# Kernel optimization log

Hardware: AMD Instinct MI355X
Metric: run time of the kernel (lower is better)

The kernel has to match this reference:

```python
import jax, jax.numpy as jnp
import numpy as np

B, L, DI = 256, 64, 2048   # batch, image regions, image feature dim
T, DT = 32, 512            # caption length, text embedding dim
U, A = 512, 512            # GRU units, attention units


def setup_inputs() -> dict:
    key = jax.random.key(0)
    ks = jax.random.split(key, 14)
    s = 0.02
    return {
        "img": jax.random.normal(ks[0], (B, L, DI), jnp.float32),
        "text": jax.random.normal(ks[1], (B, T, DT), jnp.float32),
        "kernel": jax.random.normal(ks[2], (DI + DT, 3 * U), jnp.float32) * s,
        "input_bias": jax.random.normal(ks[3], (3 * U,), jnp.float32) * s,
        "recurrent_kernel": jax.random.normal(ks[4], (U, 3 * U), jnp.float32) * s,
        "recurrent_bias": jax.random.normal(ks[5], (3 * U,), jnp.float32) * s,
        "att_img_kernel": jax.random.normal(ks[6], (DI, A), jnp.float32) * s,
        "att_img_bias": jax.random.normal(ks[7], (A,), jnp.float32) * s,
        "att_hidden_kernel": jax.random.normal(ks[8], (U, A), jnp.float32) * s,
        "att_hidden_bias": jax.random.normal(ks[9], (A,), jnp.float32) * s,
        "att_v_kernel": jax.random.normal(ks[10], (A, 1), jnp.float32) * s,
        "att_v_bias": jax.random.normal(ks[11], (1,), jnp.float32) * s,
    }


def reference(img, text, kernel, input_bias, recurrent_kernel, recurrent_bias,
              att_img_kernel, att_img_bias, att_hidden_kernel, att_hidden_bias,
              att_v_kernel, att_v_bias):
    # Precompute the image attention projection (independent of h; the
    # original recomputes it each step, but the math is identical).
    img_proj = jnp.einsum('bld,da->bla', img, att_img_kernel) + att_img_bias  # [B,L,A]

    def step(h, x_t):
        # Bahdanau attention over image regions
        hid = jnp.tanh(img_proj + (h @ att_hidden_kernel + att_hidden_bias)[:, None, :])  # [B,L,A]
        score = hid @ att_v_kernel + att_v_bias                # [B,L,1]
        attw = jax.nn.softmax(score, axis=1)                   # softmax over regions
        ctx = jnp.sum(attw * img, axis=1)                      # [B,DI]
        # GRU gate math (keras GRU v2 convention, reset gate applied after matmul)
        inp = jnp.concatenate([x_t, ctx], axis=-1)             # [B,DT+DI]
        mx = inp @ kernel + input_bias                         # [B,3U]
        mi = h @ recurrent_kernel + recurrent_bias             # [B,3U]
        x_z, x_r, x_h = jnp.split(mx, 3, axis=-1)
        r_z, r_r, r_h = jnp.split(mi, 3, axis=-1)
        z = jax.nn.sigmoid(x_z + r_z)
        r = jax.nn.sigmoid(x_r + r_r)
        hh = jnp.tanh(x_h + r * r_h)
        h_new = z * h + (1.0 - z) * hh
        return h_new, h_new

    h0 = jnp.zeros((img.shape[0], recurrent_kernel.shape[0]), img.dtype)
    _, seq = jax.lax.scan(step, h0, jnp.swapaxes(text, 0, 1))  # seq: [T,B,U]
    return jnp.swapaxes(seq, 0, 1)                             # [B,T,U]
```

## Files before the change

kernel.cpp:

```cpp
#include <hip/hip_runtime.h>
#include <hip/hip_bf16.h>

#define B_  256
#define L_  64
#define DI_ 2048
#define T_  32
#define DT_ 512
#define U_  512
#define A_  512
#define N3U 1536

typedef short short8 __attribute__((ext_vector_type(8)));
typedef float floatx4 __attribute__((ext_vector_type(4)));

__device__ __forceinline__ unsigned short f2bf(float f) {
  unsigned int u = __float_as_uint(f);
  u += 0x7fffu + ((u >> 16) & 1u);
  return (unsigned short)(u >> 16);
}
__device__ __forceinline__ float bf2f(unsigned short s) {
  return __uint_as_float(((unsigned int)s) << 16);
}
__device__ __forceinline__ float fast_tanh(float x) {
  x = fminf(fmaxf(x, -15.f), 15.f);
  float e = __expf(2.f * x);
  return (e - 1.f) / (e + 1.f);
}

__global__ __launch_bounds__(256) void gemm_a32_bt16_mfma(
    const float* __restrict__ A, const unsigned short* __restrict__ Bt,
    const float* __restrict__ bias, void* __restrict__ Cout,
    int M, int N, int K, int out_bf16) {
  __shared__ unsigned short As[128][40];
  __shared__ unsigned short Bs[128][40];
  const int tid  = threadIdx.x;
  const int wave = tid >> 6;
  const int lane = tid & 63;
  const int quad = lane >> 4;
  const int lr   = lane & 15;
  const int wrow = (wave >> 1) * 64;
  const int wcol = (wave & 1) * 64;
  const size_t bm = (size_t)blockIdx.y * 128;
  const size_t bn = (size_t)blockIdx.x * 128;

  const int sr = tid >> 2;
  const int sc = (tid & 3) * 8;

  floatx4 acc[4][4] = {};

  for (int k0 = 0; k0 < K; k0 += 32) {
#pragma unroll
    for (int it = 0; it < 2; ++it) {
      const int row = sr + it * 64;
      const float* ap = A + (bm + row) * (size_t)K + k0 + sc;
      float4 a0 = *(const float4*)(ap);
      float4 a1 = *(const float4*)(ap + 4);
      short8 pk;
      pk[0] = (short)f2bf(a0.x); pk[1] = (short)f2bf(a0.y);
      pk[2] = (short)f2bf(a0.z); pk[3] = (short)f2bf(a0.w);
      pk[4] = (short)f2bf(a1.x); pk[5] = (short)f2bf(a1.y);
      pk[6] = (short)f2bf(a1.z); pk[7] = (short)f2bf(a1.w);
      *(short8*)&As[row][sc] = pk;
      *(float4*)&Bs[row][sc] = *(const float4*)(Bt + (bn + row) * (size_t)K + k0 + sc);
    }
    __syncthreads();
    short8 af[4], bf[4];
#pragma unroll
    for (int mi = 0; mi < 4; ++mi) af[mi] = *(const short8*)&As[wrow + mi * 16 + lr][quad * 8];
#pragma unroll
    for (int ni = 0; ni < 4; ++ni) bf[ni] = *(const short8*)&Bs[wcol + ni * 16 + lr][quad * 8];
#pragma unroll
    for (int mi = 0; mi < 4; ++mi)
#pragma unroll
      for (int ni = 0; ni < 4; ++ni)
        acc[mi][ni] = __builtin_amdgcn_mfma_f32_16x16x32_bf16(af[mi], bf[ni], acc[mi][ni], 0, 0, 0);
    __syncthreads();
  }

  float* outf = (float*)Cout;
  unsigned short* outb = (unsigned short*)Cout;
#pragma unroll
  for (int mi = 0; mi < 4; ++mi) {
#pragma unroll
    for (int ni = 0; ni < 4; ++ni) {
      const size_t row0 = bm + wrow + mi * 16 + quad * 4;
      const size_t col  = bn + wcol + ni * 16 + lr;
      const float bsum = bias ? bias[col] : 0.f;
#pragma unroll
      for (int reg = 0; reg < 4; ++reg) {
        const float v = acc[mi][ni][reg] + bsum;
        if (out_bf16) outb[(row0 + reg) * (size_t)N + col] = f2bf(v);
        else          outf[(row0 + reg) * (size_t)N + col] = v;
      }
    }
  }
}

__global__ void zero_f32(float* __restrict__ p, int n) {
  int i = blockIdx.x * 256 + threadIdx.x;
  if (i < n) p[i] = 0.f;
}

__global__ __launch_bounds__(256) void transpose_f32_bf16(
    const float* __restrict__ in, unsigned short* __restrict__ outp, int K, int N) {
  __shared__ unsigned short tile[32][33];
  const int tid = threadIdx.x;
  const int tx = tid & 31, ty = tid >> 5;
  const int k0 = blockIdx.y * 32, n0 = blockIdx.x * 32;
#pragma unroll
  for (int i = 0; i < 4; ++i) {
    const int kk = ty + i * 8;
    tile[tx][kk] = f2bf(in[(size_t)(k0 + kk) * N + n0 + tx]);
  }
  __syncthreads();
#pragma unroll
  for (int i = 0; i < 4; ++i) {
    const int nn = ty + i * 8;
    outp[(size_t)(n0 + nn) * K + k0 + tx] = tile[nn][tx];
  }
}

__global__ void build_bcat(const float* __restrict__ ahb,
                           const float* __restrict__ rb,
                           float* __restrict__ bcat) {
  int i = blockIdx.x * 256 + threadIdx.x;
  if (i < A_) bcat[i] = ahb[i];
  else if (i < A_ + N3U) bcat[i] = rb[i - A_];
}

__global__ __launch_bounds__(512) void attn_gru_step(
    const unsigned short* __restrict__ img_proj,
    const unsigned short* __restrict__ imgW,
    const float* __restrict__ text_proj,
    const float* __restrict__ hm,
    const float* __restrict__ vk,
    float* __restrict__ h,
    float* __restrict__ out,
    int t) {
  const int b = blockIdx.x;
  const int tid = threadIdx.x;
  const int lane = tid & 63;
  const int wave = tid >> 6;
  __shared__ float sc[L_];
  __shared__ float aw[L_];

  const float* hpg = hm + (size_t)b * 2048;
  float hpv[8], vvv[8];
  {
    float4 h0 = *(const float4*)(hpg + lane * 8);
    float4 h1 = *(const float4*)(hpg + lane * 8 + 4);
    float4 v0 = *(const float4*)(vk + lane * 8);
    float4 v1 = *(const float4*)(vk + lane * 8 + 4);
    hpv[0]=h0.x; hpv[1]=h0.y; hpv[2]=h0.z; hpv[3]=h0.w;
    hpv[4]=h1.x; hpv[5]=h1.y; hpv[6]=h1.z; hpv[7]=h1.w;
    vvv[0]=v0.x; vvv[1]=v0.y; vvv[2]=v0.z; vvv[3]=v0.w;
    vvv[4]=v1.x; vvv[5]=v1.y; vvv[6]=v1.z; vvv[7]=v1.w;
  }

#pragma unroll
  for (int i = 0; i < 8; ++i) {
    const int l = wave + i * 8;
    const unsigned short* ip = img_proj + ((size_t)b * L_ + l) * A_ + lane * 8;
    short8 v8 = *(const short8*)ip;
    float s = 0.f;
#pragma unroll
    for (int j = 0; j < 8; ++j) {
      s += fast_tanh(bf2f((unsigned short)v8[j]) + hpv[j]) * vvv[j];
    }
#pragma unroll
    for (int off = 32; off; off >>= 1) s += __shfl_down(s, off);
    if (lane == 0) sc[l] = s;
  }
  __syncthreads();

  if (tid < 64) {
    float x = sc[tid];
    float m = x;
#pragma unroll
    for (int off = 32; off; off >>= 1) m = fmaxf(m, __shfl_xor(m, off));
    float e = __expf(x - m);
    float ssum = e;
#pragma unroll
    for (int off = 32; off; off >>= 1) ssum += __shfl_xor(ssum, off);
    aw[tid] = e / ssum;
  }
  __syncthreads();

  const int u = tid;
  const unsigned short* iw = imgW + (size_t)b * L_ * N3U + u;
  float s0 = 0.f, s1 = 0.f, s2 = 0.f;
#pragma unroll 8
  for (int l = 0; l < L_; ++l) {
    const float a = aw[l];
    const unsigned short* p = iw + l * N3U;
    s0 += a * bf2f(p[0]);
    s1 += a * bf2f(p[512]);
    s2 += a * bf2f(p[1024]);
  }
  const float* tp  = text_proj + ((size_t)b * T_ + t) * N3U;
  const float* mib = hm + (size_t)b * 2048 + 512;
  const float xz = s0 + tp[u]        + mib[u];
  const float xr = s1 + tp[512 + u]  + mib[512 + u];
  const float xh = s2 + tp[1024 + u];
  const float rh = mib[1024 + u];
  const float z = 1.f / (1.f + __expf(-xz));
  const float r = 1.f / (1.f + __expf(-xr));
  const float hh = fast_tanh(xh + r * rh);
  const float hn = z * h[b * U_ + u] + (1.f - z) * hh;
  h[b * U_ + u] = hn;
  out[((size_t)b * T_ + t) * U_ + u] = hn;
}

extern "C" void kernel_launch(void* const* d_in, const int* in_sizes, int n_in,
                              void* d_out, int out_size, void* d_ws, size_t ws_size,
                              hipStream_t stream) {
  const float* img        = (const float*)d_in[0];
  const float* text       = (const float*)d_in[1];
  const float* kern       = (const float*)d_in[2];
  const float* input_bias = (const float*)d_in[3];
  const float* rec_kern   = (const float*)d_in[4];
  const float* rec_bias   = (const float*)d_in[5];
  const float* att_img_k  = (const float*)d_in[6];
  const float* att_img_b  = (const float*)d_in[7];
  const float* att_hid_k  = (const float*)d_in[8];
  const float* att_hid_b  = (const float*)d_in[9];
  const float* att_v_k    = (const float*)d_in[10];
  float* out = (float*)d_out;

  char* ws = (char*)d_ws;
  size_t off = 0;
  auto alloc = [&](size_t bytes) { char* p = ws + off; off += (bytes + 255) & ~(size_t)255; return p; };
  unsigned short* img_proj = (unsigned short*)alloc((size_t)B_*L_*A_*2);
  unsigned short* imgW     = (unsigned short*)alloc((size_t)B_*L_*N3U*2);
  float*          text_proj= (float*)         alloc((size_t)B_*T_*N3U*4);
  unsigned short* wt1      = (unsigned short*)alloc((size_t)A_*DI_*2);
  unsigned short* wt2      = (unsigned short*)alloc((size_t)N3U*DI_*2);
  unsigned short* wt3      = (unsigned short*)alloc((size_t)N3U*DT_*2);
  unsigned short* wcatT    = (unsigned short*)alloc((size_t)2048*U_*2);
  float*          bcat     = (float*)         alloc(2048*4);
  float*          h        = (float*)         alloc((size_t)B_*U_*4);
  float*          hm       = (float*)         alloc((size_t)B_*2048*4);

  dim3 blk(256);

  zero_f32<<<dim3((B_*U_ + 255) / 256), blk, 0, stream>>>(h, B_*U_);

  transpose_f32_bf16<<<dim3(A_/32, DI_/32), blk, 0, stream>>>(att_img_k, wt1, DI_, A_);
  transpose_f32_bf16<<<dim3(N3U/32, DI_/32), blk, 0, stream>>>(kern + (size_t)DT_*N3U, wt2, DI_, N3U);
  transpose_f32_bf16<<<dim3(N3U/32, DT_/32), blk, 0, stream>>>(kern, wt3, DT_, N3U);
  transpose_f32_bf16<<<dim3(A_/32, U_/32), blk, 0, stream>>>(att_hid_k, wcatT, U_, A_);
  transpose_f32_bf16<<<dim3(N3U/32, U_/32), blk, 0, stream>>>(rec_kern, wcatT + (size_t)A_*U_, U_, N3U);
  build_bcat<<<dim3(8), blk, 0, stream>>>(att_hid_b, rec_bias, bcat);

  gemm_a32_bt16_mfma<<<dim3(A_/128, (B_*L_)/128), blk, 0, stream>>>(
      img, wt1, att_img_b, img_proj, B_*L_, A_, DI_, 1);
  gemm_a32_bt16_mfma<<<dim3(N3U/128, (B_*L_)/128), blk, 0, stream>>>(
      img, wt2, nullptr, imgW, B_*L_, N3U, DI_, 1);
  gemm_a32_bt16_mfma<<<dim3(N3U/128, (B_*T_)/128), blk, 0, stream>>>(
      text, wt3, input_bias, text_proj, B_*T_, N3U, DT_, 0);

  for (int t = 0; t < T_; ++t) {
    gemm_a32_bt16_mfma<<<dim3(2048/128, B_/128), blk, 0, stream>>>(
        h, wcatT, bcat, hm, B_, 2048, U_, 0);
    attn_gru_step<<<dim3(B_), dim3(512), 0, stream>>>(
        img_proj, imgW, text_proj, hm, att_v_k, h, out, t);
  }
}
```

Baseline: 1.770 ms.

## Fuse recurrent loop into one persistent cooperative kernel with grid syncs

Replaces the 64 per-step launches (recurrent GEMM plus attention/GRU step) with a single cooperative kernel of 256 blocks that loops over time. Each block computes one tile of the h-projection GEMM with MFMA, then all blocks grid-sync before doing the attention and GRU update. The imgW projection is also written in an interleaved 8-row layout so the context reduction can use vector loads. This removes kernel launch overhead and per-step GEMM tiling inefficiency, but adds two grid-wide barriers per step and relies on all 256 blocks being co-resident.

```diff
diff --git a/kernel.cpp b/kernel.cpp
--- a/kernel.cpp
+++ b/kernel.cpp
@@ -1,5 +1,7 @@
 #include <hip/hip_runtime.h>
-#include <hip/hip_bf16.h>
+#include <hip/hip_cooperative_groups.h>
+
+namespace cg = cooperative_groups;
 
 #define B_  256
 #define L_  64
@@ -12,6 +14,7 @@
 
 typedef short short8 __attribute__((ext_vector_type(8)));
 typedef float floatx4 __attribute__((ext_vector_type(4)));
+typedef unsigned short ushort4v __attribute__((ext_vector_type(4)));
 
 __device__ __forceinline__ unsigned short f2bf(float f) {
   unsigned int u = __float_as_uint(f);
@@ -30,7 +33,7 @@
 __global__ __launch_bounds__(256) void gemm_a32_bt16_mfma(
     const float* __restrict__ A, const unsigned short* __restrict__ Bt,
     const float* __restrict__ bias, void* __restrict__ Cout,
-    int M, int N, int K, int out_bf16) {
+    int M, int N, int K, int out_mode) {
   __shared__ unsigned short As[128][40];
   __shared__ unsigned short Bs[128][40];
   const int tid  = threadIdx.x;
@@ -86,19 +89,24 @@
       const size_t row0 = bm + wrow + mi * 16 + quad * 4;
       const size_t col  = bn + wcol + ni * 16 + lr;
       const float bsum = bias ? bias[col] : 0.f;
-#pragma unroll
-      for (int reg = 0; reg < 4; ++reg) {
-        const float v = acc[mi][ni][reg] + bsum;
-        if (out_bf16) outb[(row0 + reg) * (size_t)N + col] = f2bf(v);
-        else          outf[(row0 + reg) * (size_t)N + col] = v;
+      if (out_mode == 2) {
+        const size_t bidx = row0 >> 6;
+        const int l0 = (int)(row0 & 63);
+        const int j = l0 >> 3, i0 = l0 & 7;
+        ushort4v pk;
+#pragma unroll
+        for (int reg = 0; reg < 4; ++reg) pk[reg] = f2bf(acc[mi][ni][reg] + bsum);
+        *(ushort4v*)(outb + (((bidx * 8 + j) * 1536 + col) << 3) + i0) = pk;
+      } else {
+#pragma unroll
+        for (int reg = 0; reg < 4; ++reg) {
+          const float v = acc[mi][ni][reg] + bsum;
+          if (out_mode == 1) outb[(row0 + reg) * (size_t)N + col] = f2bf(v);
+          else               outf[(row0 + reg) * (size_t)N + col] = v;
+        }
       }
     }
   }
-}
-
-__global__ void zero_f32(float* __restrict__ p, int n) {
-  int i = blockIdx.x * 256 + threadIdx.x;
-  if (i < n) p[i] = 0.f;
 }
 
 __global__ __launch_bounds__(256) void transpose_f32_bf16(
@@ -128,87 +136,145 @@
   else if (i < A_ + N3U) bcat[i] = rb[i - A_];
 }
 
-__global__ __launch_bounds__(512) void attn_gru_step(
+__global__ __launch_bounds__(512) void recurrence(
     const unsigned short* __restrict__ img_proj,
-    const unsigned short* __restrict__ imgW,
+    const unsigned short* __restrict__ imgW8,
     const float* __restrict__ text_proj,
-    const float* __restrict__ hm,
+    const unsigned short* __restrict__ wcatT,
+    const float* __restrict__ bcat,
     const float* __restrict__ vk,
     float* __restrict__ h,
-    float* __restrict__ out,
-    int t) {
-  const int b = blockIdx.x;
-  const int tid = threadIdx.x;
+    float* __restrict__ hm,
+    float* __restrict__ out) {
+  cg::grid_group grid = cg::this_grid();
+  const int tid  = threadIdx.x;
+  const int bid  = blockIdx.x;
+  const int wave = tid >> 6;
   const int lane = tid & 63;
-  const int wave = tid >> 6;
+  const int quad = lane >> 4;
+  const int lr   = lane & 15;
+  const int b    = bid;
+
+  __shared__ unsigned short As[32][520];
   __shared__ float sc[L_];
   __shared__ float aw[L_];
 
-  const float* hpg = hm + (size_t)b * 2048;
-  float hpv[8], vvv[8];
+  h[(size_t)bid * U_ + tid] = 0.f;
+
+  float vvv[8];
   {
-    float4 h0 = *(const float4*)(hpg + lane * 8);
-    float4 h1 = *(const float4*)(hpg + lane * 8 + 4);
     float4 v0 = *(const float4*)(vk + lane * 8);
     float4 v1 = *(const float4*)(vk + lane * 8 + 4);
-    hpv[0]=h0.x; hpv[1]=h0.y; hpv[2]=h0.z; hpv[3]=h0.w;
-    hpv[4]=h1.x; hpv[5]=h1.y; hpv[6]=h1.z; hpv[7]=h1.w;
     vvv[0]=v0.x; vvv[1]=v0.y; vvv[2]=v0.z; vvv[3]=v0.w;
     vvv[4]=v1.x; vvv[5]=v1.y; vvv[6]=v1.z; vvv[7]=v1.w;
   }
 
-#pragma unroll
-  for (int i = 0; i < 8; ++i) {
-    const int l = wave + i * 8;
-    const unsigned short* ip = img_proj + ((size_t)b * L_ + l) * A_ + lane * 8;
-    short8 v8 = *(const short8*)ip;
-    float s = 0.f;
+  const int mt   = bid & 7;
+  const int nt   = bid >> 3;
+  const int mrow = (wave >> 2) * 16;
+  const int ncol = nt * 64 + (wave & 3) * 16;
+
+  grid.sync();
+
+  for (int t = 0; t < T_; ++t) {
+    {
+      const int r  = tid >> 4;
+      const int c0 = (tid & 15) << 5;
+      const float* hp = h + (size_t)(mt * 32 + r) * U_ + c0;
+#pragma unroll
+      for (int i = 0; i < 4; ++i) {
+        float4 x0 = *(const float4*)(hp + i * 8);
+        float4 x1 = *(const float4*)(hp + i * 8 + 4);
+        short8 pk;
+        pk[0] = (short)f2bf(x0.x); pk[1] = (short)f2bf(x0.y);
+        pk[2] = (short)f2bf(x0.z); pk[3] = (short)f2bf(x0.w);
+        pk[4] = (short)f2bf(x1.x); pk[5] = (short)f2bf(x1.y);
+        pk[6] = (short)f2bf(x1.z); pk[7] = (short)f2bf(x1.w);
+        *(short8*)&As[r][c0 + i * 8] = pk;
+      }
+      __syncthreads();
+      floatx4 acc = {};
+#pragma unroll
+      for (int k0 = 0; k0 < U_; k0 += 32) {
+        short8 af  = *(const short8*)&As[mrow + lr][k0 + quad * 8];
+        short8 bfr = *(const short8*)(wcatT + (size_t)(ncol + lr) * U_ + k0 + quad * 8);
+        acc = __builtin_amdgcn_mfma_f32_16x16x32_bf16(af, bfr, acc, 0, 0, 0);
+      }
+      const int col  = ncol + lr;
+      const float bs = bcat[col];
+      const int orow = mt * 32 + mrow + quad * 4;
+#pragma unroll
+      for (int reg = 0; reg < 4; ++reg)
+        hm[(size_t)(orow + reg) * 2048 + col] = acc[reg] + bs;
+    }
+    grid.sync();
+
+    const float* hpg = hm + (size_t)b * 2048;
+    float hpv[8];
+    {
+      float4 h0 = *(const float4*)(hpg + lane * 8);
+      float4 h1 = *(const float4*)(hpg + lane * 8 + 4);
+      hpv[0]=h0.x; hpv[1]=h0.y; hpv[2]=h0.z; hpv[3]=h0.w;
+      hpv[4]=h1.x; hpv[5]=h1.y; hpv[6]=h1.z; hpv[7]=h1.w;
+    }
+#pragma unroll
+    for (int i = 0; i < 8; ++i) {
+      const int l = wave + i * 8;
+      const unsigned short* ip = img_proj + ((size_t)b * L_ + l) * A_ + lane * 8;
+      short8 v8 = *(const short8*)ip;
+      float s = 0.f;
+#pragma unroll
+      for (int j = 0; j < 8; ++j)
+        s += fast_tanh(bf2f((unsigned short)v8[j]) + hpv[j]) * vvv[j];
+#pragma unroll
+      for (int off = 32; off; off >>= 1) s += __shfl_down(s, off);
+      if (lane == 0) sc[l] = s;
+    }
+    __syncthreads();
+    if (tid < 64) {
+      float x = sc[tid];
+      float m = x;
+#pragma unroll
+      for (int off = 32; off; off >>= 1) m = fmaxf(m, __shfl_xor(m, off));
+      float e = __expf(x - m);
+      float ssum = e;
+#pragma unroll
+      for (int off = 32; off; off >>= 1) ssum += __shfl_xor(ssum, off);
+      aw[tid] = e / ssum;
+    }
+    __syncthreads();
+
+    const int u = tid;
+    const unsigned short* iwb = imgW8 + (size_t)b * 8 * (N3U * 8) + (size_t)u * 8;
+    float s0 = 0.f, s1 = 0.f, s2 = 0.f;
 #pragma unroll
     for (int j = 0; j < 8; ++j) {
-      s += fast_tanh(bf2f((unsigned short)v8[j]) + hpv[j]) * vvv[j];
-    }
-#pragma unroll
-    for (int off = 32; off; off >>= 1) s += __shfl_down(s, off);
-    if (lane == 0) sc[l] = s;
-  }
-  __syncthreads();
-
-  if (tid < 64) {
-    float x = sc[tid];
-    float m = x;
-#pragma unroll
-    for (int off = 32; off; off >>= 1) m = fmaxf(m, __shfl_xor(m, off));
-    float e = __expf(x - m);
-    float ssum = e;
-#pragma unroll
-    for (int off = 32; off; off >>= 1) ssum += __shfl_xor(ssum, off);
-    aw[tid] = e / ssum;
-  }
-  __syncthreads();
-
-  const int u = tid;
-  const unsigned short* iw = imgW + (size_t)b * L_ * N3U + u;
-  float s0 = 0.f, s1 = 0.f, s2 = 0.f;
-#pragma unroll 8
-  for (int l = 0; l < L_; ++l) {
-    const float a = aw[l];
-    const unsigned short* p = iw + l * N3U;
-    s0 += a * bf2f(p[0]);
-    s1 += a * bf2f(p[512]);
-    s2 += a * bf2f(p[1024]);
-  }
-  const float* tp  = text_proj + ((size_t)b * T_ + t) * N3U;
-  const float* mib = hm + (size_t)b * 2048 + 512;
-  const float xz = s0 + tp[u]        + mib[u];
-  const float xr = s1 + tp[512 + u]  + mib[512 + u];
-  const float xh = s2 + tp[1024 + u];
-  const float rh = mib[1024 + u];
-  const float z = 1.f / (1.f + __expf(-xz));
-  const float r = 1.f / (1.f + __expf(-xr));
-  const float hh = fast_tanh(xh + r * rh);
-  const float hn = z * h[b * U_ + u] + (1.f - z) * hh;
-  h[b * U_ + u] = hn;
-  out[((size_t)b * T_ + t) * U_ + u] = hn;
+      const unsigned short* pj = iwb + (size_t)j * (N3U * 8);
+      short8 v0 = *(const short8*)(pj);
+      short8 v1 = *(const short8*)(pj + 512 * 8);
+      short8 v2 = *(const short8*)(pj + 1024 * 8);
+#pragma unroll
+      for (int i = 0; i < 8; ++i) {
+        const float a = aw[j * 8 + i];
+        s0 += a * bf2f((unsigned short)v0[i]);
+        s1 += a * bf2f((unsigned short)v1[i]);
+        s2 += a * bf2f((unsigned short)v2[i]);
+      }
+    }
+    const float* tp  = text_proj + ((size_t)b * T_ + t) * N3U;
+    const float* mib = hpg + 512;
+    const float xz = s0 + tp[u]        + mib[u];
+    const float xr = s1 + tp[512 + u]  + mib[512 + u];
+    const float xh = s2 + tp[1024 + u];
+    const float rh = mib[1024 + u];
+    const float z  = 1.f / (1.f + __expf(-xz));
+    const float r  = 1.f / (1.f + __expf(-xr));
+    const float hh = fast_tanh(xh + r * rh);
+    const float hn = z * h[(size_t)b * U_ + u] + (1.f - z) * hh;
+    h[(size_t)b * U_ + u] = hn;
+    out[((size_t)b * T_ + t) * U_ + u] = hn;
+    grid.sync();
+  }
 }
 
 extern "C" void kernel_launch(void* const* d_in, const int* in_sizes, int n_in,
@@ -231,7 +297,7 @@
   size_t off = 0;
   auto alloc = [&](size_t bytes) { char* p = ws + off; off += (bytes + 255) & ~(size_t)255; return p; };
   unsigned short* img_proj = (unsigned short*)alloc((size_t)B_*L_*A_*2);
-  unsigned short* imgW     = (unsigned short*)alloc((size_t)B_*L_*N3U*2);
+  unsigned short* imgW8    = (unsigned short*)alloc((size_t)B_*L_*N3U*2);
   float*          text_proj= (float*)         alloc((size_t)B_*T_*N3U*4);
   unsigned short* wt1      = (unsigned short*)alloc((size_t)A_*DI_*2);
   unsigned short* wt2      = (unsigned short*)alloc((size_t)N3U*DI_*2);
@@ -243,8 +309,6 @@
 
   dim3 blk(256);
 
-  zero_f32<<<dim3((B_*U_ + 255) / 256), blk, 0, stream>>>(h, B_*U_);
-
   transpose_f32_bf16<<<dim3(A_/32, DI_/32), blk, 0, stream>>>(att_img_k, wt1, DI_, A_);
   transpose_f32_bf16<<<dim3(N3U/32, DI_/32), blk, 0, stream>>>(kern + (size_t)DT_*N3U, wt2, DI_, N3U);
   transpose_f32_bf16<<<dim3(N3U/32, DT_/32), blk, 0, stream>>>(kern, wt3, DT_, N3U);
@@ -255,14 +319,14 @@
   gemm_a32_bt16_mfma<<<dim3(A_/128, (B_*L_)/128), blk, 0, stream>>>(
       img, wt1, att_img_b, img_proj, B_*L_, A_, DI_, 1);
   gemm_a32_bt16_mfma<<<dim3(N3U/128, (B_*L_)/128), blk, 0, stream>>>(
-      img, wt2, nullptr, imgW, B_*L_, N3U, DI_, 1);
+      img, wt2, nullptr, imgW8, B_*L_, N3U, DI_, 2);
   gemm_a32_bt16_mfma<<<dim3(N3U/128, (B_*T_)/128), blk, 0, stream>>>(
       text, wt3, input_bias, text_proj, B_*T_, N3U, DT_, 0);
 
-  for (int t = 0; t < T_; ++t) {
-    gemm_a32_bt16_mfma<<<dim3(2048/128, B_/128), blk, 0, stream>>>(
-        h, wcatT, bcat, hm, B_, 2048, U_, 0);
-    attn_gru_step<<<dim3(B_), dim3(512), 0, stream>>>(
-        img_proj, imgW, text_proj, hm, att_v_k, h, out, t);
-  }
-}
+  void* kargs[] = {
+    (void*)&img_proj, (void*)&imgW8, (void*)&text_proj, (void*)&wcatT,
+    (void*)&bcat, (void*)&att_v_k, (void*)&h, (void*)&hm, (void*)&out
+  };
+  hipLaunchCooperativeKernel((const void*)recurrence, dim3(256), dim3(512),
+                             kargs, 0, stream);
+}
```

New measurement: 3.605 ms. 2.04x slower.
